# Kernel optimization log

Measured on AMD Instinct MI355X. Metric: run time of the kernel, lower is better.

## Reference

```python
import jax, jax.numpy as jnp
import numpy as np

ATT = 512  # attention_size

def setup_inputs() -> dict:
    key = jax.random.key(0)
    k0, k1, k2, k3, k4 = jax.random.split(key, 5)
    B, Sq, Sk, Din, Dmem = 32, 1024, 1024, 512, 512
    inputs = jax.random.normal(k0, (B, Sq, Din), dtype=jnp.float32)
    memory = jax.random.normal(k1, (B, Sk, Dmem), dtype=jnp.float32)
    memory_mask = jax.random.randint(k2, (B, Sk), 0, 2).astype(jnp.int32)
    W_input = (jax.random.normal(k3, (Din, ATT), dtype=jnp.float32) * 0.02)
    W_memory = (jax.random.normal(k4, (Dmem, ATT), dtype=jnp.float32) * 0.02)
    return {"inputs": inputs, "memory": memory, "memory_mask": memory_mask,
            "W_input": W_input, "W_memory": W_memory}

def reference(inputs, memory, memory_mask, W_input, W_memory):
    # projections (bias=False) + ReLU; dropout=0 -> identity
    x = jax.nn.relu(jnp.einsum('bqd,da->bqa', inputs, W_input))   # [B,Sq,A]
    m = jax.nn.relu(jnp.einsum('bkd,da->bka', memory, W_memory))  # [B,Sk,A]
    scale = 1.0 / jnp.sqrt(jnp.asarray(ATT, dtype=inputs.dtype))
    logits = jnp.einsum('bqa,bka->bqk', x, m) * scale             # [B,Sq,Sk]
    mask = (memory_mask[:, None, :] != 0)                         # [B,1,Sk] broadcast over Sq
    logits = jnp.where(mask, logits, jnp.asarray(-1e30, dtype=logits.dtype))
    score = jax.nn.softmax(logits, axis=-1)
    context = jnp.einsum('bqk,bkd->bqd', score, memory)           # [B,Sq,Dmem]
    return jnp.concatenate([context, inputs], axis=-1)            # [B,Sq,Dmem+Din]
```

## Files before the change

### kernel.cpp

```cpp
#include <hip/hip_runtime.h>

typedef __bf16 bf16x8 __attribute__((ext_vector_type(8)));
typedef float f32x4 __attribute__((ext_vector_type(4)));

__device__ __forceinline__ unsigned short f2bf(float f) {
    union { float f; unsigned u; } v; v.f = f;
    unsigned r = v.u + 0x7FFFu + ((v.u >> 16) & 1u);
    return (unsigned short)(r >> 16);
}

__global__ __launch_bounds__(256) void prep_kernel(
    const float4* __restrict__ inputs4, uint2* __restrict__ InB16,
    float4* __restrict__ out4,
    const float* __restrict__ W0, const float* __restrict__ W1,
    unsigned short* __restrict__ D0, unsigned short* __restrict__ D1,
    const int* __restrict__ mask,
    int* __restrict__ cnt, int* __restrict__ padded,
    float4* __restrict__ rowsum4,
    const float* __restrict__ memory,
    unsigned short* __restrict__ MemG, unsigned short* __restrict__ MemGT)
{
    __shared__ float tile[32][33];
    __shared__ float tileG[32][132];
    __shared__ int wsum[4];
    __shared__ int kidx32[32];
    const int bid = blockIdx.x;
    const int t = threadIdx.x;

    if (bid < 1024) {
        const int b = bid >> 5;
        const int jt = bid & 31;
        const int j0 = jt * 32;
        const int* m = mask + b * 1024;
        int v[4]; int s = 0;
#pragma unroll
        for (int e = 0; e < 4; e++) { v[e] = (m[t * 4 + e] != 0) ? 1 : 0; s += v[e]; }
        const int lane = t & 63, wv = t >> 6;
        int x = s;
#pragma unroll
        for (int off = 1; off < 64; off <<= 1) {
            int y = __shfl_up(x, off, 64);
            if (lane >= off) x += y;
        }
        if (lane == 63) wsum[wv] = x;
        __syncthreads();
        int base = 0;
        for (int w = 0; w < wv; w++) base += wsum[w];
        const int nb = wsum[0] + wsum[1] + wsum[2] + wsum[3];
        const int pb = (nb + 127) & ~127;
        if (j0 >= pb) return;
        int pos = base + x - s;
#pragma unroll
        for (int e = 0; e < 4; e++)
            if (v[e]) {
                int p = pos++;
                if (p >= j0 && p < j0 + 32) kidx32[p - j0] = t * 4 + e;
            }
        __syncthreads();

        const float4* src4 = (const float4*)(memory + (size_t)b * 1024 * 512);
        const int jj = t >> 3;
        const int cq = t & 7;
        const bool live = (j0 + jj) < nb;
        const int krow = live ? kidx32[jj] : 0;

        float4 vv[4][4];
        if (live) {
            const float4* rp = src4 + (size_t)krow * 128 + cq * 4;
#pragma unroll
            for (int c = 0; c < 4; c++)
#pragma unroll
                for (int i = 0; i < 4; i++) vv[c][i] = rp[c * 32 + i];
        } else {
#pragma unroll
            for (int c = 0; c < 4; c++)
#pragma unroll
                for (int i = 0; i < 4; i++) vv[c][i] = float4{0.f, 0.f, 0.f, 0.f};
        }

        unsigned short* mg = MemG + (size_t)b * 1024 * 512 + (size_t)(j0 + jj) * 512;
#pragma unroll
        for (int c = 0; c < 4; c++) {
            union { unsigned short u[16]; uint4 q[2]; } pk;
#pragma unroll
            for (int i = 0; i < 4; i++) {
                pk.u[i * 4 + 0] = f2bf(vv[c][i].x); pk.u[i * 4 + 1] = f2bf(vv[c][i].y);
                pk.u[i * 4 + 2] = f2bf(vv[c][i].z); pk.u[i * 4 + 3] = f2bf(vv[c][i].w);
            }
            *(uint4*)&mg[c * 128 + cq * 16] = pk.q[0];
            *(uint4*)&mg[c * 128 + cq * 16 + 8] = pk.q[1];
        }

        const int dd = t >> 1;
        const int jh = (t & 1) * 16;
        unsigned short* gtb = MemGT + (size_t)b * 512 * 1024 + j0 + jh;
#pragma unroll
        for (int c = 0; c < 4; c++) {
#pragma unroll
            for (int i = 0; i < 4; i++)
                *(float4*)&tileG[jj][cq * 16 + i * 4] = vv[c][i];
            __syncthreads();
            union { unsigned short u[16]; uint4 q[2]; } pt;
#pragma unroll
            for (int k = 0; k < 16; k++) pt.u[k] = f2bf(tileG[jh + k][dd]);
            unsigned short* gt = gtb + (size_t)(c * 128 + dd) * 1024;
            *(uint4*)&gt[0] = pt.q[0];
            *(uint4*)&gt[8] = pt.q[1];
            __syncthreads();
        }
    } else if (bid < 1056) {
        const int b = bid - 1024;
        rowsum4[b * 256 + t] = float4{0.f, 0.f, 0.f, 0.f};
        const int* m = mask + b * 1024;
        int s = 0;
#pragma unroll
        for (int e = 0; e < 4; e++) s += (m[t * 4 + e] != 0) ? 1 : 0;
        const int lane = t & 63, wv = t >> 6;
        int x = s;
#pragma unroll
        for (int off = 1; off < 64; off <<= 1) {
            int y = __shfl_up(x, off, 64);
            if (lane >= off) x += y;
        }
        if (lane == 63) wsum[wv] = x;
        __syncthreads();
        if (t == 255) {
            int total = wsum[0] + wsum[1] + wsum[2] + wsum[3];
            cnt[b] = total;
            padded[b] = (total + 127) & ~127;
        }
    } else if (bid < 1568) {
        const int tb = bid - 1056;
        const float* src = (tb >> 8) ? W1 : W0;
        unsigned short* dst = (tb >> 8) ? D1 : D0;
        const int rem = tb & 255;
        const int s0 = (rem & 15) * 32, d0 = (rem >> 4) * 32;
        const int tr = t >> 5, tc = t & 31;
#pragma unroll
        for (int i = 0; i < 4; i++)
            tile[tr + i * 8][tc] = src[(size_t)(s0 + tr + i * 8) * 512 + d0 + tc];
        __syncthreads();
#pragma unroll
        for (int i = 0; i < 4; i++)
            dst[(size_t)(d0 + tr + i * 8) * 512 + s0 + tc] = f2bf(tile[tc][tr + i * 8]);
    } else {
        const int i = (bid - 1568) * 256 + t;
        const int bq = i >> 7;
        const int d  = i & 127;
        float4 v = inputs4[i];
        out4[(size_t)bq * 256 + 128 + d] = v;
        union { unsigned short u[4]; uint2 p; } pk;
        pk.u[0] = f2bf(v.x); pk.u[1] = f2bf(v.y);
        pk.u[2] = f2bf(v.z); pk.u[3] = f2bf(v.w);
        InB16[i] = pk.p;
    }
}

template<int CMODE>
__device__ __forceinline__ void gemm_core(
    unsigned char* lds,
    const unsigned short* __restrict__ Ab, const unsigned short* __restrict__ Bb,
    void* __restrict__ Cb, float* __restrict__ rs, int nbv,
    int rowA, int rowB, int Kz, int lda, int ldb, int ldc, float scale)
{
    const int nt = Kz >> 6;

    const int t = threadIdx.x;
    const int w = t >> 6;
    const int lane = t & 63;
    const int wm = w >> 1;
    const int wn = w & 1;
    const int l15 = lane & 15;
    const int sx = (((lane >> 4) ^ ((l15 >> 1) & 3)) << 4);

    const int r0 = t >> 2;
    const int sl = (t & 3) ^ ((t >> 3) & 3);
    const unsigned short* aS0 = Ab + (size_t)(rowA + r0) * lda + sl * 8;
    const unsigned short* aS1 = aS0 + (size_t)64 * lda;
    const unsigned short* bS0 = Bb + (size_t)(rowB + r0) * ldb + sl * 8;
    const unsigned short* bS1 = bS0 + (size_t)64 * ldb;

    const int wofs = w * 1024;
    const int aRd = (wm * 64 + l15) * 64 + sx;
    const int bRd = 16384 + (wn * 64 + l15) * 64 + sx;

    f32x4 acc[4][4];
#pragma unroll
    for (int i = 0; i < 4; i++)
#pragma unroll
        for (int j = 0; j < 4; j++) acc[i][j] = f32x4{0.f, 0.f, 0.f, 0.f};

#define GLL(SRC, DOFS) __builtin_amdgcn_global_load_lds(                        \
        (const __attribute__((address_space(1))) void*)(SRC),                   \
        (__attribute__((address_space(3))) void*)&lds[DOFS], 16, 0, 0)
#define STAGEA(BUF, KH, KEL) do {                                               \
        GLL(aS0 + (KEL), (BUF) * 32768 + (KH) * 8192 + wofs);                   \
        GLL(aS1 + (KEL), (BUF) * 32768 + (KH) * 8192 + wofs + 4096); } while (0)
#define STAGEB(BUF, KH, KEL) do {                                               \
        GLL(bS0 + (KEL), (BUF) * 32768 + 16384 + (KH) * 8192 + wofs);           \
        GLL(bS1 + (KEL), (BUF) * 32768 + 16384 + (KH) * 8192 + wofs + 4096); } while (0)

    STAGEA(0, 0, 0); STAGEB(0, 0, 0); STAGEA(0, 1, 32); STAGEB(0, 1, 32);
    asm volatile("s_waitcnt vmcnt(4)" ::: "memory");
    __builtin_amdgcn_s_barrier();

    for (int tt = 0; tt < nt; ++tt) {
        const int cur = (tt & 1) * 32768;
        const int nxt = (tt & 1) ^ 1;
        const bool pf = (tt + 1) < nt;
        const int kn = (tt + 1) * 64;
        bf16x8 af[4], bfr[4];

#pragma unroll
        for (int i = 0; i < 4; i++) af[i]  = *(const bf16x8*)&lds[cur + aRd + i * 1024];
#pragma unroll
        for (int j = 0; j < 4; j++) bfr[j] = *(const bf16x8*)&lds[cur + bRd + j * 1024];
        if (pf) { STAGEA(nxt, 0, kn); STAGEB(nxt, 0, kn); }
        __builtin_amdgcn_s_barrier();
        asm volatile("s_waitcnt lgkmcnt(0)" ::: "memory");
        __builtin_amdgcn_sched_barrier(0);
        __builtin_amdgcn_s_setprio(1);
#pragma unroll
        for (int i = 0; i < 4; i++)
#pragma unroll
            for (int j = 0; j < 4; j++)
                acc[i][j] = __builtin_amdgcn_mfma_f32_16x16x32_bf16(af[i], bfr[j], acc[i][j], 0, 0, 0);
        __builtin_amdgcn_s_setprio(0);
        if (pf) { asm volatile("s_waitcnt vmcnt(4)" ::: "memory"); }
        else    { asm volatile("s_waitcnt vmcnt(0)" ::: "memory"); }
        __builtin_amdgcn_s_barrier();

#pragma unroll
        for (int i = 0; i < 4; i++) af[i]  = *(const bf16x8*)&lds[cur + 8192 + aRd + i * 1024];
#pragma unroll
        for (int j = 0; j < 4; j++) bfr[j] = *(const bf16x8*)&lds[cur + 8192 + bRd + j * 1024];
        if (pf) { STAGEA(nxt, 1, kn + 32); STAGEB(nxt, 1, kn + 32); }
        __builtin_amdgcn_s_barrier();
        asm volatile("s_waitcnt lgkmcnt(0)" ::: "memory");
        __builtin_amdgcn_sched_barrier(0);
        __builtin_amdgcn_s_setprio(1);
#pragma unroll
        for (int i = 0; i < 4; i++)
#pragma unroll
            for (int j = 0; j < 4; j++)
                acc[i][j] = __builtin_amdgcn_mfma_f32_16x16x32_bf16(af[i], bfr[j], acc[i][j], 0, 0, 0);
        __builtin_amdgcn_s_setprio(0);
        if (pf) { asm volatile("s_waitcnt vmcnt(4)" ::: "memory"); }
        __builtin_amdgcn_s_barrier();
    }

#undef GLL
#undef STAGEA
#undef STAGEB

    const int orow = (lane >> 4) * 4;
    const int ocol = l15;

    if constexpr (CMODE == 0) {
        unsigned short* C = (unsigned short*)Cb;
#pragma unroll
        for (int mf = 0; mf < 4; mf++)
#pragma unroll
            for (int nf = 0; nf < 4; nf++) {
                const int col = rowB + wn * 64 + nf * 16 + ocol;
#pragma unroll
                for (int r = 0; r < 4; r++) {
                    const int rw = rowA + wm * 64 + mf * 16 + orow + r;
                    C[(size_t)rw * ldc + col] = f2bf(fmaxf(acc[mf][nf][r], 0.f));
                }
            }
    } else if constexpr (CMODE == 1) {
        unsigned short* C = (unsigned short*)Cb;
#pragma unroll
        for (int mf = 0; mf < 4; mf++) {
            float part[4] = {0.f, 0.f, 0.f, 0.f};
#pragma unroll
            for (int nf = 0; nf < 4; nf++) {
                const int col = rowB + wn * 64 + nf * 16 + ocol;
#pragma unroll
                for (int r = 0; r < 4; r++) {
                    float p = (col < nbv) ? __expf(acc[mf][nf][r] * scale) : 0.f;
                    part[r] += p;
                    const int rw = rowA + wm * 64 + mf * 16 + orow + r;
                    C[(size_t)rw * ldc + col] = f2bf(p);
                }
            }
#pragma unroll
            for (int r = 0; r < 4; r++) {
                float s = part[r];
                s += __shfl_xor(s, 1, 64);
                s += __shfl_xor(s, 2, 64);
                s += __shfl_xor(s, 4, 64);
                s += __shfl_xor(s, 8, 64);
                if (ocol == 0)
                    atomicAdd(&rs[rowA + wm * 64 + mf * 16 + orow + r], s);
            }
        }
    } else {
        float* C = (float*)Cb;
#pragma unroll
        for (int mf = 0; mf < 4; mf++) {
            float inv[4];
#pragma unroll
            for (int r = 0; r < 4; r++)
                inv[r] = 1.0f / rs[rowA + wm * 64 + mf * 16 + orow + r];
#pragma unroll
            for (int nf = 0; nf < 4; nf++) {
                const int col = rowB + wn * 64 + nf * 16 + ocol;
#pragma unroll
                for (int r = 0; r < 4; r++) {
                    const int rw = rowA + wm * 64 + mf * 16 + orow + r;
                    C[(size_t)rw * ldc + col] = acc[mf][nf][r] * inv[r];
                }
            }
        }
    }
}

__global__ __launch_bounds__(256, 2) void gemm_proj_kernel(
    const unsigned short* __restrict__ InB16, const unsigned short* __restrict__ WtIn,
    unsigned short* __restrict__ Xq,
    const unsigned short* __restrict__ MemG, const unsigned short* __restrict__ WtMem,
    unsigned short* __restrict__ Xm, const int* __restrict__ padded)
{
    __shared__ __align__(16) unsigned char lds[65536];
    const int id = blockIdx.x;
    const int xcd = id & 7, u8 = id >> 3;
    const int y = xcd + 8 * (u8 >> 2);
    const int x = u8 & 3;
    const int rowB = x * 128;
    const unsigned short* A;
    const unsigned short* Bt;
    unsigned short* C;
    int rowA;
    if (y < 256) {
        A = InB16; Bt = WtIn; C = Xq; rowA = y * 128;
    } else {
        const int idx = y - 256;
        const int z = idx >> 3;
        rowA = (idx & 7) * 128;
        if (rowA >= padded[z]) return;
        A = MemG + (size_t)z * 524288;
        Bt = WtMem;
        C = Xm + (size_t)z * 524288;
    }
    gemm_core<0>(lds, A, Bt, (void*)C, nullptr, 0, rowA, rowB,
                 512, 512, 512, 512, 0.f);
}

__global__ __launch_bounds__(256, 2) void gemm_p_kernel(
    const unsigned short* __restrict__ Xq, const unsigned short* __restrict__ Xm,
    unsigned short* __restrict__ P, const int* __restrict__ cnt,
    const int* __restrict__ padded, float* __restrict__ rowsum, float scale)
{
    __shared__ __align__(16) unsigned char lds[65536];
    const int id = blockIdx.x;
    const int xcd = id & 7, u = id >> 3;
    const int z = xcd + 8 * (u >> 6);
    const int r = u & 63;
    const int x = r & 7, y = r >> 3;
    const int rowB = x * 128;
    if (rowB >= padded[z]) return;
    gemm_core<1>(lds, Xq + (size_t)z * 524288, Xm + (size_t)z * 524288,
                 (void*)(P + (size_t)z * 1048576), rowsum + (size_t)z * 1024, cnt[z],
                 y * 128, rowB, 512, 512, 512, 1024, scale);
}

__global__ __launch_bounds__(256, 2) void gemm_ctx_kernel(
    const unsigned short* __restrict__ P, const unsigned short* __restrict__ MemGT,
    float* __restrict__ out, const int* __restrict__ padded, float* __restrict__ rowsum)
{
    __shared__ __align__(16) unsigned char lds[65536];
    const int id = blockIdx.x;
    const int xcd = id & 7, u = id >> 3;
    const int z = xcd + 8 * (u >> 5);
    const int r = u & 31;
    const int x = r & 3, y = r >> 2;
    gemm_core<2>(lds, P + (size_t)z * 1048576, MemGT + (size_t)z * 524288,
                 (void*)(out + (size_t)z * 1048576), rowsum + (size_t)z * 1024, 0,
                 y * 128, x * 128, padded[z],
                 1024, 1024, 1024, 1.f);
}

extern "C" void kernel_launch(void* const* d_in, const int* in_sizes, int n_in,
                              void* d_out, int out_size, void* d_ws, size_t ws_size,
                              hipStream_t stream)
{
    const float* inputs = (const float*)d_in[0];
    const float* memory = (const float*)d_in[1];
    const int*   mmask  = (const int*)d_in[2];
    const float* W_in   = (const float*)d_in[3];
    const float* W_mem  = (const float*)d_in[4];
    float* out = (float*)d_out;

    char* ws = (char*)d_ws;
    const unsigned long long MB = 1048576ull;
    unsigned short* Wt_in  = (unsigned short*)(ws);
    unsigned short* Wt_mem = (unsigned short*)(ws + 524288);
    unsigned short* InB16  = (unsigned short*)(ws + 1 * MB);
    unsigned short* MemG   = (unsigned short*)(ws + 33 * MB);
    unsigned short* P      = (unsigned short*)(ws + 1 * MB);
    unsigned short* MemGT  = (unsigned short*)(ws + 65 * MB);
    unsigned short* Xq     = (unsigned short*)(ws + 97 * MB);
    unsigned short* Xm     = (unsigned short*)(ws + 129 * MB);
    float*          rowsum = (float*)(ws + 161 * MB);
    int*            cntp   = (int*)(ws + 161 * MB + 262144);
    int*            padp   = (int*)(ws + 161 * MB + 262144 + 128);

    const float scale = 0.04419417382415922f;

    prep_kernel<<<17952, 256, 0, stream>>>(
        (const float4*)inputs, (uint2*)InB16, (float4*)out,
        W_in, W_mem, Wt_in, Wt_mem,
        mmask, cntp, padp, (float4*)rowsum,
        memory, MemG, MemGT);

    gemm_proj_kernel<<<2048, 256, 0, stream>>>(
        InB16, Wt_in, Xq, MemG, Wt_mem, Xm, padp);

    gemm_p_kernel<<<2048, 256, 0, stream>>>(
        Xq, Xm, P, cntp, padp, rowsum, scale);

    gemm_ctx_kernel<<<1024, 256, 0, stream>>>(
        P, MemGT, out, padp, rowsum);
}
```

Baseline: 366.8 us.

## Fuse score GEMM, softmax and context GEMM into one flash-style attention kernel

Replaces the separate P-score GEMM and context GEMM kernels with a single fused kernel. Each block handles 64 query rows, computes exp-scores per 64-key tile into LDS and immediately multiplies them by memory to accumulate context, normalizing at the end with a block-local row sum. This removes the bf16 P matrix round-trip through global memory, the rowsum atomics and its zeroing, and one launch. In exchange, grid size drops to 512 blocks with large per-thread accumulators. B fragments are loaded straight from global memory without LDS staging, so latency hiding and occupancy may suffer.

```diff
diff --git a/kernel.cpp b/kernel.cpp
--- a/kernel.cpp
+++ b/kernel.cpp
@@ -16,7 +16,6 @@
     unsigned short* __restrict__ D0, unsigned short* __restrict__ D1,
     const int* __restrict__ mask,
     int* __restrict__ cnt, int* __restrict__ padded,
-    float4* __restrict__ rowsum4,
     const float* __restrict__ memory,
     unsigned short* __restrict__ MemG, unsigned short* __restrict__ MemGT)
 {
@@ -110,7 +109,6 @@
         }
     } else if (bid < 1056) {
         const int b = bid - 1024;
-        rowsum4[b * 256 + t] = float4{0.f, 0.f, 0.f, 0.f};
         const int* m = mask + b * 1024;
         int s = 0;
 #pragma unroll
@@ -156,12 +154,11 @@
     }
 }
 
-template<int CMODE>
-__device__ __forceinline__ void gemm_core(
+__device__ __forceinline__ void gemm_core0(
     unsigned char* lds,
     const unsigned short* __restrict__ Ab, const unsigned short* __restrict__ Bb,
-    void* __restrict__ Cb, float* __restrict__ rs, int nbv,
-    int rowA, int rowB, int Kz, int lda, int ldb, int ldc, float scale)
+    unsigned short* __restrict__ C,
+    int rowA, int rowB, int Kz, int lda, int ldb, int ldc)
 {
     const int nt = Kz >> 6;
 
@@ -255,66 +252,17 @@
 
     const int orow = (lane >> 4) * 4;
     const int ocol = l15;
-
-    if constexpr (CMODE == 0) {
-        unsigned short* C = (unsigned short*)Cb;
-#pragma unroll
-        for (int mf = 0; mf < 4; mf++)
-#pragma unroll
-            for (int nf = 0; nf < 4; nf++) {
-                const int col = rowB + wn * 64 + nf * 16 + ocol;
-#pragma unroll
-                for (int r = 0; r < 4; r++) {
-                    const int rw = rowA + wm * 64 + mf * 16 + orow + r;
-                    C[(size_t)rw * ldc + col] = f2bf(fmaxf(acc[mf][nf][r], 0.f));
-                }
-            }
-    } else if constexpr (CMODE == 1) {
-        unsigned short* C = (unsigned short*)Cb;
-#pragma unroll
-        for (int mf = 0; mf < 4; mf++) {
-            float part[4] = {0.f, 0.f, 0.f, 0.f};
-#pragma unroll
-            for (int nf = 0; nf < 4; nf++) {
-                const int col = rowB + wn * 64 + nf * 16 + ocol;
-#pragma unroll
-                for (int r = 0; r < 4; r++) {
-                    float p = (col < nbv) ? __expf(acc[mf][nf][r] * scale) : 0.f;
-                    part[r] += p;
-                    const int rw = rowA + wm * 64 + mf * 16 + orow + r;
-                    C[(size_t)rw * ldc + col] = f2bf(p);
-                }
-            }
+#pragma unroll
+    for (int mf = 0; mf < 4; mf++)
+#pragma unroll
+        for (int nf = 0; nf < 4; nf++) {
+            const int col = rowB + wn * 64 + nf * 16 + ocol;
 #pragma unroll
             for (int r = 0; r < 4; r++) {
-                float s = part[r];
-                s += __shfl_xor(s, 1, 64);
-                s += __shfl_xor(s, 2, 64);
-                s += __shfl_xor(s, 4, 64);
-                s += __shfl_xor(s, 8, 64);
-                if (ocol == 0)
-                    atomicAdd(&rs[rowA + wm * 64 + mf * 16 + orow + r], s);
-            }
-        }
-    } else {
-        float* C = (float*)Cb;
-#pragma unroll
-        for (int mf = 0; mf < 4; mf++) {
-            float inv[4];
-#pragma unroll
-            for (int r = 0; r < 4; r++)
-                inv[r] = 1.0f / rs[rowA + wm * 64 + mf * 16 + orow + r];
-#pragma unroll
-            for (int nf = 0; nf < 4; nf++) {
-                const int col = rowB + wn * 64 + nf * 16 + ocol;
-#pragma unroll
-                for (int r = 0; r < 4; r++) {
-                    const int rw = rowA + wm * 64 + mf * 16 + orow + r;
-                    C[(size_t)rw * ldc + col] = acc[mf][nf][r] * inv[r];
-                }
-            }
-        }
-    }
+                const int rw = rowA + wm * 64 + mf * 16 + orow + r;
+                C[(size_t)rw * ldc + col] = f2bf(fmaxf(acc[mf][nf][r], 0.f));
+            }
+        }
 }
 
 __global__ __launch_bounds__(256, 2) void gemm_proj_kernel(
@@ -344,42 +292,155 @@
         Bt = WtMem;
         C = Xm + (size_t)z * 524288;
     }
-    gemm_core<0>(lds, A, Bt, (void*)C, nullptr, 0, rowA, rowB,
-                 512, 512, 512, 512, 0.f);
-}
-
-__global__ __launch_bounds__(256, 2) void gemm_p_kernel(
+    gemm_core0(lds, A, Bt, C, rowA, rowB, 512, 512, 512, 512);
+}
+
+__global__ __launch_bounds__(256, 2) void fused_attn_kernel(
     const unsigned short* __restrict__ Xq, const unsigned short* __restrict__ Xm,
-    unsigned short* __restrict__ P, const int* __restrict__ cnt,
-    const int* __restrict__ padded, float* __restrict__ rowsum, float scale)
+    const unsigned short* __restrict__ MemGT, float* __restrict__ out,
+    const int* __restrict__ cnt, const int* __restrict__ padded, float scale)
 {
-    __shared__ __align__(16) unsigned char lds[65536];
+    __shared__ __align__(16) unsigned char lds[73984];
     const int id = blockIdx.x;
     const int xcd = id & 7, u = id >> 3;
-    const int z = xcd + 8 * (u >> 6);
-    const int r = u & 63;
-    const int x = r & 7, y = r >> 3;
-    const int rowB = x * 128;
-    if (rowB >= padded[z]) return;
-    gemm_core<1>(lds, Xq + (size_t)z * 524288, Xm + (size_t)z * 524288,
-                 (void*)(P + (size_t)z * 1048576), rowsum + (size_t)z * 1024, cnt[z],
-                 y * 128, rowB, 512, 512, 512, 1024, scale);
-}
-
-__global__ __launch_bounds__(256, 2) void gemm_ctx_kernel(
-    const unsigned short* __restrict__ P, const unsigned short* __restrict__ MemGT,
-    float* __restrict__ out, const int* __restrict__ padded, float* __restrict__ rowsum)
-{
-    __shared__ __align__(16) unsigned char lds[65536];
-    const int id = blockIdx.x;
-    const int xcd = id & 7, u = id >> 3;
-    const int z = xcd + 8 * (u >> 5);
-    const int r = u & 31;
-    const int x = r & 3, y = r >> 2;
-    gemm_core<2>(lds, P + (size_t)z * 1048576, MemGT + (size_t)z * 524288,
-                 (void*)(out + (size_t)z * 1048576), rowsum + (size_t)z * 1024, 0,
-                 y * 128, x * 128, padded[z],
-                 1024, 1024, 1024, 1.f);
+    const int z = xcd + 8 * (u >> 4);
+    const int q0 = (u & 15) * 64;
+    const int cz = cnt[z];
+    const int nkt = padded[z] >> 6;
+
+    const int t = threadIdx.x;
+    const int w = t >> 6;
+    const int lane = t & 63;
+    const int g = lane >> 4;
+    const int l15 = lane & 15;
+
+    const unsigned short* XqZ = Xq + (size_t)z * 524288 + (size_t)q0 * 512;
+    const unsigned short* XmZ = Xm + (size_t)z * 524288;
+    const unsigned short* GTZ = MemGT + (size_t)z * 524288;
+    float* outZ = out + (size_t)z * 1048576 + (size_t)q0 * 1024;
+
+    const int srow = t >> 4;
+    const int sslot = (t & 15) ^ srow;
+
+    f32x4 acc[4][8];
+#pragma unroll
+    for (int i = 0; i < 4; i++)
+#pragma unroll
+        for (int j = 0; j < 8; j++) acc[i][j] = f32x4{0.f, 0.f, 0.f, 0.f};
+    f32x4 s[4];
+#pragma unroll
+    for (int i = 0; i < 4; i++) s[i] = f32x4{0.f, 0.f, 0.f, 0.f};
+    float rsum = 0.f;
+
+#define GLL(SRC, DOFS) __builtin_amdgcn_global_load_lds(                        \
+        (const __attribute__((address_space(1))) void*)(SRC),                   \
+        (__attribute__((address_space(3))) void*)&lds[DOFS], 16, 0, 0)
+#define STAGE_XMQ(BUF, KT, KK) do {                                             \
+        _Pragma("unroll")                                                       \
+        for (int i_ = 0; i_ < 4; i_++) {                                        \
+            GLL(XmZ + (size_t)((KT) * 64 + i_ * 16 + srow) * 512 + (KK) * 128 + sslot * 8, \
+                (BUF) * 16384 + i_ * 4096 + t * 16);                            \
+            GLL(XqZ + (size_t)(i_ * 16 + srow) * 512 + (KK) * 128 + sslot * 8,  \
+                32768 + (BUF) * 16384 + i_ * 4096 + t * 16);                    \
+        } } while (0)
+
+    if (nkt > 0) STAGE_XMQ(0, 0, 0);
+
+    for (int kt = 0; kt < nkt; ++kt) {
+#pragma unroll 1
+        for (int kk = 0; kk < 4; ++kk) {
+            const int bcur = (kk & 1) * 16384;
+            if (kk < 3) {
+                STAGE_XMQ((kk + 1) & 1, kt, kk + 1);
+                asm volatile("s_waitcnt vmcnt(8)" ::: "memory");
+            } else {
+                asm volatile("s_waitcnt vmcnt(0)" ::: "memory");
+            }
+            __builtin_amdgcn_s_barrier();
+            __builtin_amdgcn_s_setprio(1);
+#pragma unroll
+            for (int c = 0; c < 4; c++) {
+                const int so = (((g + 4 * c) ^ l15) << 4);
+                bf16x8 bq = *(const bf16x8*)&lds[32768 + bcur + (w * 16 + l15) * 256 + so];
+#pragma unroll
+                for (int i = 0; i < 4; i++) {
+                    bf16x8 am = *(const bf16x8*)&lds[bcur + (i * 16 + l15) * 256 + so];
+                    s[i] = __builtin_amdgcn_mfma_f32_16x16x32_bf16(am, bq, s[i], 0, 0, 0);
+                }
+            }
+            __builtin_amdgcn_s_setprio(0);
+            __builtin_amdgcn_s_barrier();
+        }
+
+        {
+            const int q = w * 16 + l15;
+            const int kbase = kt * 64 + g * 4;
+#pragma unroll
+            for (int t4 = 0; t4 < 4; t4++) {
+                float p0 = (kbase + t4 * 16 + 0 < cz) ? __expf(s[t4][0] * scale) : 0.f;
+                float p1 = (kbase + t4 * 16 + 1 < cz) ? __expf(s[t4][1] * scale) : 0.f;
+                float p2 = (kbase + t4 * 16 + 2 < cz) ? __expf(s[t4][2] * scale) : 0.f;
+                float p3 = (kbase + t4 * 16 + 3 < cz) ? __expf(s[t4][3] * scale) : 0.f;
+                rsum += (p0 + p1) + (p2 + p3);
+                unsigned lo = (unsigned)f2bf(p0) | ((unsigned)f2bf(p1) << 16);
+                unsigned hi = (unsigned)f2bf(p2) | ((unsigned)f2bf(p3) << 16);
+                const int base = 65536 + q * 128 +
+                    (((2 * t4 + (g >> 1)) ^ (q & 7)) << 4) + ((g & 1) << 3);
+                *(unsigned*)&lds[base]     = lo;
+                *(unsigned*)&lds[base + 4] = hi;
+                s[t4] = f32x4{0.f, 0.f, 0.f, 0.f};
+            }
+        }
+        __syncthreads();
+
+        if (kt + 1 < nkt) STAGE_XMQ(0, kt + 1, 0);
+#pragma unroll
+        for (int kc = 0; kc < 2; kc++) {
+            bf16x8 A[4], B[8];
+#pragma unroll
+            for (int qt = 0; qt < 4; qt++)
+                A[qt] = *(const bf16x8*)&lds[65536 + (qt * 16 + l15) * 128 +
+                                             ((((kc << 2) + g) ^ (l15 & 7)) << 4)];
+            const unsigned short* gb = GTZ + (size_t)(w * 128 + l15) * 1024 +
+                                       kt * 64 + kc * 32 + g * 8;
+#pragma unroll
+            for (int dt = 0; dt < 8; dt++)
+                B[dt] = *(const bf16x8*)(gb + (size_t)dt * 16 * 1024);
+            __builtin_amdgcn_s_setprio(1);
+#pragma unroll
+            for (int qt = 0; qt < 4; qt++)
+#pragma unroll
+                for (int dt = 0; dt < 8; dt++)
+                    acc[qt][dt] = __builtin_amdgcn_mfma_f32_16x16x32_bf16(
+                        A[qt], B[dt], acc[qt][dt], 0, 0, 0);
+            __builtin_amdgcn_s_setprio(0);
+        }
+        __builtin_amdgcn_s_barrier();
+    }
+#undef GLL
+#undef STAGE_XMQ
+
+    rsum += __shfl_xor(rsum, 16, 64);
+    rsum += __shfl_xor(rsum, 32, 64);
+    if (lane < 16) *(float*)&lds[73728 + (w * 16 + l15) * 4] = rsum;
+    __syncthreads();
+
+#pragma unroll
+    for (int qt = 0; qt < 4; qt++) {
+        const f32x4 rsv = *(const f32x4*)&lds[73728 + (qt * 16 + g * 4) * 4];
+        float ir[4];
+#pragma unroll
+        for (int r = 0; r < 4; r++) ir[r] = 1.0f / rsv[r];
+#pragma unroll
+        for (int dt = 0; dt < 8; dt++) {
+            const int d = w * 128 + dt * 16 + l15;
+#pragma unroll
+            for (int r = 0; r < 4; r++) {
+                const int q = qt * 16 + g * 4 + r;
+                outZ[(size_t)q * 1024 + d] = acc[qt][dt][r] * ir[r];
+            }
+        }
+    }
 }
 
 extern "C" void kernel_launch(void* const* d_in, const int* in_sizes, int n_in,
@@ -399,11 +460,9 @@
     unsigned short* Wt_mem = (unsigned short*)(ws + 524288);
     unsigned short* InB16  = (unsigned short*)(ws + 1 * MB);
     unsigned short* MemG   = (unsigned short*)(ws + 33 * MB);
-    unsigned short* P      = (unsigned short*)(ws + 1 * MB);
     unsigned short* MemGT  = (unsigned short*)(ws + 65 * MB);
     unsigned short* Xq     = (unsigned short*)(ws + 97 * MB);
     unsigned short* Xm     = (unsigned short*)(ws + 129 * MB);
-    float*          rowsum = (float*)(ws + 161 * MB);
     int*            cntp   = (int*)(ws + 161 * MB + 262144);
     int*            padp   = (int*)(ws + 161 * MB + 262144 + 128);
 
@@ -412,15 +471,12 @@
     prep_kernel<<<17952, 256, 0, stream>>>(
         (const float4*)inputs, (uint2*)InB16, (float4*)out,
         W_in, W_mem, Wt_in, Wt_mem,
-        mmask, cntp, padp, (float4*)rowsum,
+        mmask, cntp, padp,
         memory, MemG, MemGT);
 
     gemm_proj_kernel<<<2048, 256, 0, stream>>>(
         InB16, Wt_in, Xq, MemG, Wt_mem, Xm, padp);
 
-    gemm_p_kernel<<<2048, 256, 0, stream>>>(
-        Xq, Xm, P, cntp, padp, rowsum, scale);
-
-    gemm_ctx_kernel<<<1024, 256, 0, stream>>>(
-        P, MemGT, out, padp, rowsum);
-}
+    fused_attn_kernel<<<512, 256, 0, stream>>>(
+        Xq, Xm, MemGT, out, cntp, padp, scale);
+}
```

Measured after the change: 374.0 us. No clear change (+2.0%).
